# Kernel tuning notes

Hardware: AMD Instinct MI355X
Metric: run time of the kernel (lower is better)

## Reference

```python
import jax, jax.numpy as jnp
import numpy as np

C = 256
NH, NL, NP_ = 8, 3, 4
HD = C // NH
NLAYERS = 6


def sine_pos(H, W, num_feats=128, temperature=10000.0, eps=1e-6):
    # mmdet SinePositionalEncoding with normalize=True and an all-zero padding mask:
    # cumsum of ones -> (i+1), normalized by last element (H or W) * 2*pi.
    scale = 2.0 * np.pi
    y = (jnp.arange(1, H + 1, dtype=jnp.float32) / (H + eps)) * scale
    x = (jnp.arange(1, W + 1, dtype=jnp.float32) / (W + eps)) * scale
    d = jnp.arange(num_feats, dtype=jnp.float32)
    dim_t = temperature ** (2.0 * jnp.floor(d / 2.0) / num_feats)

    def interleave(p):  # p: (n, num_feats) -> sin on even dims, cos on odd dims, interleaved
        return jnp.stack([jnp.sin(p[:, 0::2]), jnp.cos(p[:, 1::2])], axis=-1).reshape(p.shape[0], -1)

    py = interleave(y[:, None] / dim_t)  # (H, num_feats)
    px = interleave(x[:, None] / dim_t)  # (W, num_feats)
    pos = jnp.concatenate([jnp.broadcast_to(py[:, None, :], (H, W, num_feats)),
                           jnp.broadcast_to(px[None, :, :], (H, W, num_feats))], axis=-1)
    return pos.reshape(H * W, 2 * num_feats)


def ref_points(H, W):
    # normalized pixel centers, (x, y) order, shape (H*W, 2)
    ry = (jnp.arange(H, dtype=jnp.float32) + 0.5) / H
    rx = (jnp.arange(W, dtype=jnp.float32) + 0.5) / W
    gy, gx = jnp.meshgrid(ry, rx, indexing='ij')
    return jnp.stack([gx.ravel(), gy.ravel()], axis=-1)


def ln(x, w, b, eps=1e-5):
    m = x.mean(-1, keepdims=True)
    v = x.var(-1, keepdims=True)
    return (x - m) / jnp.sqrt(v + eps) * w + b


def gnorm(x, w, b, groups=32, eps=1e-5):
    B, Ch, H, W = x.shape
    xg = x.reshape(B, groups, Ch // groups, H, W)
    m = xg.mean((2, 3, 4), keepdims=True)
    v = xg.var((2, 3, 4), keepdims=True)
    xg = (xg - m) / jnp.sqrt(v + eps)
    return xg.reshape(B, Ch, H, W) * w[None, :, None, None] + b[None, :, None, None]


def conv3x3(x, w):
    return jax.lax.conv_general_dilated(x, w, (1, 1), 'SAME',
                                        dimension_numbers=('NCHW', 'OIHW', 'NCHW'))


def ms_deform(value, shapes, loc, aw):
    # value (B,S,NH,HD); loc (B,L,NH,NL,NP,2) normalized [0,1]; aw (B,L,NH,NL,NP)
    # Matches F.grid_sample(..., align_corners=False, padding_mode='zeros').
    B, S, nH, hd = value.shape
    Lq, nP = loc.shape[1], loc.shape[4]
    out = jnp.zeros((B, Lq, nH, hd), value.dtype)
    start = 0
    for lvl, (H, W) in enumerate(shapes):
        v = value[:, start:start + H * W].transpose(0, 2, 1, 3)  # (B,nH,HW,hd)
        start += H * W
        l = loc[:, :, :, lvl]                 # (B,Lq,nH,nP,2)
        px = l[..., 0] * W - 0.5
        py = l[..., 1] * H - 0.5
        x0 = jnp.floor(px); y0 = jnp.floor(py)
        lx = px - x0; ly = py - y0
        x0i = x0.astype(jnp.int32); y0i = y0.astype(jnp.int32)

        def tw(w_):  # (B,Lq,nH,nP) -> (B,nH,Lq*nP,1)
            return w_.transpose(0, 2, 1, 3).reshape(B, nH, Lq * nP, 1)

        def gather(xi, yi):
            valid = ((xi >= 0) & (xi < W) & (yi >= 0) & (yi < H)).astype(value.dtype)
            idx = jnp.clip(yi, 0, H - 1) * W + jnp.clip(xi, 0, W - 1)
            idx = idx.transpose(0, 2, 1, 3).reshape(B, nH, Lq * nP)
            g = jnp.take_along_axis(v, idx[..., None], axis=2)  # (B,nH,Lq*nP,hd)
            return g * tw(valid)

        samp = (gather(x0i, y0i) * tw((1 - lx) * (1 - ly))
                + gather(x0i + 1, y0i) * tw(lx * (1 - ly))
                + gather(x0i, y0i + 1) * tw((1 - lx) * ly)
                + gather(x0i + 1, y0i + 1) * tw(lx * ly))
        samp = samp.reshape(B, nH, Lq, nP, hd)
        out = out + jnp.einsum('bqhp,bhqpd->bqhd', aw[:, :, :, lvl], samp)
    return out.reshape(B, Lq, nH * hd)


def _forward(feat0, feat1, feat2, in0_w, in0_b, in1_w, in1_b, in2_w, in2_b,
             off_w, off_b, aw_w, aw_b, vp_w, vp_b, op_w, op_b,
             n1_w, n1_b, ff1_w, ff1_b, ff2_w, ff2_b, n2_w, n2_b,
             fn_w, fn_b, lat_w, lat_b, out_w, gnw, gnb):
    feats = [feat0, feat1, feat2]
    in_ws = [in0_w, in1_w, in2_w]; in_bs = [in0_b, in1_b, in2_b]
    B = feat0.shape[0]
    mlvl = [jnp.einsum('oi,bihw->bohw', w, f) + b[None, :, None, None]
            for f, w, b in zip(feats, in_ws, in_bs)]
    shapes = [(f.shape[2], f.shape[3]) for f in mlvl]
    src = jnp.concatenate([f.reshape(B, C, -1).transpose(0, 2, 1) for f in mlvl], axis=1)  # (B,L,C)
    pos = jnp.concatenate([sine_pos(H, W) for (H, W) in shapes], axis=0)[None]  # (1,L,C)
    ref = jnp.concatenate([ref_points(H, W) for (H, W) in shapes], axis=0)      # (L,2)
    L = ref.shape[0]
    ref = jnp.broadcast_to(ref[None, :, None, :], (B, L, NL, 2))
    norm = jnp.array([[w_, h_] for (h_, w_) in shapes], dtype=src.dtype)  # (NL,2) = (W,H)
    for i in range(NLAYERS):
        q = src + pos
        off = (q @ off_w[i].T + off_b[i]).reshape(B, L, NH, NL, NP_, 2)
        aw = jax.nn.softmax((q @ aw_w[i].T + aw_b[i]).reshape(B, L, NH, NL * NP_), axis=-1)
        aw = aw.reshape(B, L, NH, NL, NP_)
        value = (src @ vp_w[i].T + vp_b[i]).reshape(B, L, NH, HD)
        loc = ref[:, :, None, :, None, :] + off / norm[None, None, None, :, None, :]
        attn = ms_deform(value, shapes, loc, aw) @ op_w[i].T + op_b[i]
        src = ln(src + attn, n1_w[i], n1_b[i])
        ff = jax.nn.relu(src @ ff1_w[i].T + ff1_b[i]) @ ff2_w[i].T + ff2_b[i]
        src = ln(src + ff, n2_w[i], n2_b[i])
    src = ln(src, fn_w, fn_b)
    mems, s = [], 0
    for (H, W) in shapes:
        mems.append(src[:, s:s + H * W].transpose(0, 2, 1).reshape(B, C, H, W))
        s += H * W
    mf = jnp.einsum('oi,bihw->bohw', lat_w, mems[0]) + lat_b[None, :, None, None]
    for i in range(3):
        mf = jax.nn.relu(gnorm(conv3x3(mf, out_w[i]), gnw[i], gnb[i]))
    return (mf, mems[0], mems[1], mems[2])


def setup_inputs():
    ks = iter(jax.random.split(jax.random.key(0), 64))

    def rn(shape, s=0.02):
        return jax.random.normal(next(ks), shape, dtype=jnp.float32) * s

    return dict(
        feat0=rn((1, 256, 64, 64), 1.0),
        feat1=rn((1, 512, 32, 32), 1.0),
        feat2=rn((1, 1024, 16, 16), 1.0),
        in0_w=rn((256, 256)), in0_b=rn((256,)),
        in1_w=rn((256, 512)), in1_b=rn((256,)),
        in2_w=rn((256, 1024)), in2_b=rn((256,)),
        off_w=rn((6, 192, 256), 0.002), off_b=rn((6, 192), 0.5),
        aw_w=rn((6, 96, 256)), aw_b=jnp.zeros((6, 96), jnp.float32),
        vp_w=rn((6, 256, 256)), vp_b=rn((6, 256)),
        op_w=rn((6, 256, 256)), op_b=rn((6, 256)),
        n1_w=jnp.ones((6, 256), jnp.float32), n1_b=jnp.zeros((6, 256), jnp.float32),
        ff1_w=rn((6, 1024, 256)), ff1_b=rn((6, 1024)),
        ff2_w=rn((6, 256, 1024)), ff2_b=rn((6, 256)),
        n2_w=jnp.ones((6, 256), jnp.float32), n2_b=jnp.zeros((6, 256), jnp.float32),
        fn_w=jnp.ones((256,), jnp.float32), fn_b=jnp.zeros((256,), jnp.float32),
        lat_w=rn((256, 256)), lat_b=rn((256,)),
        out_w=rn((3, 256, 256, 3, 3)),
        gnw=jnp.ones((3, 256), jnp.float32), gnb=jnp.zeros((3, 256), jnp.float32),
    )


def reference(feat0, feat1, feat2, in0_w, in0_b, in1_w, in1_b, in2_w, in2_b,
              off_w, off_b, aw_w, aw_b, vp_w, vp_b, op_w, op_b,
              n1_w, n1_b, ff1_w, ff1_b, ff2_w, ff2_b, n2_w, n2_b,
              fn_w, fn_b, lat_w, lat_b, out_w, gnw, gnb):
    return _forward(feat0, feat1, feat2, in0_w, in0_b, in1_w, in1_b, in2_w, in2_b,
                    off_w, off_b, aw_w, aw_b, vp_w, vp_b, op_w, op_b,
                    n1_w, n1_b, ff1_w, ff1_b, ff2_w, ff2_b, n2_w, n2_b,
                    fn_w, fn_b, lat_w, lat_b, out_w, gnw, gnb)
```

## Files before the change

kernel.cpp:

```cpp
#include <hip/hip_runtime.h>
#include <math.h>

#define LTOT 5376

typedef __attribute__((ext_vector_type(8))) __bf16 bf16x8;
typedef __attribute__((ext_vector_type(4))) float f32x4;
typedef __attribute__((ext_vector_type(8))) unsigned short us8;
typedef __attribute__((ext_vector_type(4))) unsigned short us4;

static __device__ __forceinline__ float4 ld4(const float* p) { return *(const float4*)p; }

static __device__ __forceinline__ unsigned short f2bf(float f) {
    unsigned int u = __float_as_uint(f);
    return (unsigned short)((u + 0x7fffu + ((u >> 16) & 1u)) >> 16);
}
static __device__ __forceinline__ float bf2f(unsigned short s) {
    return __uint_as_float(((unsigned int)s) << 16);
}

static __device__ __forceinline__ void gl16(const unsigned short* g, unsigned short* l) {
    __builtin_amdgcn_global_load_lds(
        (const __attribute__((address_space(1))) unsigned int*)g,
        (__attribute__((address_space(3))) unsigned int*)l, 16, 0, 0);
}

__device__ __forceinline__ void gemm_core(
    const unsigned short* __restrict__ A,
    const unsigned short* __restrict__ B,
    const float* __restrict__ bias,
    float* __restrict__ C1, unsigned short* __restrict__ C2,
    const float* __restrict__ posf, unsigned short* __restrict__ qb,
    unsigned short* As, unsigned short* Bs,
    int m0, int mo0, int n0, int N, int K, int omode, int relu)
{
    const int tid  = threadIdx.x;
    const int wave = tid >> 6;
    const int lane = tid & 63;
    const int wm   = (wave >> 1) * 32;
    const int wn   = (wave & 1) * 32;
    const int fr   = lane & 15;
    const int ko   = lane >> 4;

    const int q0 = tid, q1 = tid + 256;
    const int r0 = q0 >> 3, c0v = (q0 & 7) ^ (r0 & 7);
    const int r1 = q1 >> 3, c1v = (q1 & 7) ^ (r1 & 7);
    const unsigned short* a0 = A + (size_t)(m0 + r0) * K + (c0v << 3);
    const unsigned short* a1 = A + (size_t)(m0 + r1) * K + (c1v << 3);
    int bn0 = n0 + r0; if (bn0 > N - 1) bn0 = N - 1;
    int bn1 = n0 + r1; if (bn1 > N - 1) bn1 = N - 1;
    const unsigned short* b0 = B + (size_t)bn0 * K + (c0v << 3);
    const unsigned short* b1 = B + (size_t)bn1 * K + (c1v << 3);
    const int wb = wave << 9;

    f32x4 acc[2][2] = {};
    const int nt = K >> 6;

    auto stage = [&](int buf, int t) {
        const int kof = t << 6;
        gl16(a0 + kof, As + buf * 4096 + wb);
        gl16(a1 + kof, As + buf * 4096 + 2048 + wb);
        gl16(b0 + kof, Bs + buf * 4096 + wb);
        gl16(b1 + kof, Bs + buf * 4096 + 2048 + wb);
    };

    stage(0, 0);
    stage(1, 1);
    asm volatile("s_waitcnt vmcnt(4)" ::: "memory");
    __builtin_amdgcn_s_barrier();
    __builtin_amdgcn_sched_barrier(0);

    for (int t = 0; t < nt; t++) {
        if (t + 2 < nt) stage((t + 2) % 3, t + 2);
        const unsigned short* Ab = As + (t % 3) * 4096;
        const unsigned short* Bb = Bs + (t % 3) * 4096;
        #pragma unroll
        for (int sub = 0; sub < 2; sub++) {
            bf16x8 af[2], bfr[2];
            const int kk = (sub << 2) + ko;
            #pragma unroll
            for (int i = 0; i < 2; i++) {
                int r = wm + i * 16 + fr;
                af[i] = *(const bf16x8*)&Ab[(r << 6) + ((kk ^ (r & 7)) << 3)];
                int c = wn + i * 16 + fr;
                bfr[i] = *(const bf16x8*)&Bb[(c << 6) + ((kk ^ (c & 7)) << 3)];
            }
            #pragma unroll
            for (int i = 0; i < 2; i++)
                #pragma unroll
                for (int j = 0; j < 2; j++)
                    acc[i][j] = __builtin_amdgcn_mfma_f32_16x16x32_bf16(af[i], bfr[j], acc[i][j], 0, 0, 0);
        }
        if (t + 1 < nt) {
            if (t + 2 < nt) asm volatile("s_waitcnt vmcnt(4) lgkmcnt(0)" ::: "memory");
            else            asm volatile("s_waitcnt vmcnt(0) lgkmcnt(0)" ::: "memory");
            __builtin_amdgcn_s_barrier();
            __builtin_amdgcn_sched_barrier(0);
        }
    }

    #pragma unroll
    for (int j = 0; j < 2; j++) {
        int col = n0 + wn + j * 16 + fr;
        if (col >= N) continue;
        float cb = bias[col];
        #pragma unroll
        for (int i = 0; i < 2; i++) {
            #pragma unroll
            for (int r = 0; r < 4; r++) {
                int row = mo0 + wm + i * 16 + ko * 4 + r;
                float v = acc[i][j][r] + cb;
                if (relu) v = fmaxf(v, 0.f);
                size_t off = (size_t)row * N + col;
                if (omode == 0)      C1[off] = v;
                else if (omode == 1) C2[off] = f2bf(v);
                else if (omode == 2) { C1[off] = v; C2[off] = f2bf(v); }
                else { C1[off] = v; C2[off] = f2bf(v); qb[off] = f2bf(v + posf[off]); }
            }
        }
    }
}

__global__ __launch_bounds__(256) void bgemm_k(
    const unsigned short* __restrict__ A, const unsigned short* __restrict__ B,
    const float* __restrict__ bias, float* __restrict__ C1, unsigned short* __restrict__ C2,
    int N, int K, int omode, int relu)
{
    __shared__ unsigned short As[3 * 4096], Bs[3 * 4096];
    int m = blockIdx.y * 64;
    gemm_core(A, B, bias, C1, C2, nullptr, nullptr, As, Bs, m, m, blockIdx.x * 64, N, K, omode, relu);
}

__global__ __launch_bounds__(256) void oavp_k(
    const unsigned short* __restrict__ qbb, const unsigned short* __restrict__ woa,
    const float* __restrict__ boa, float* __restrict__ oab,
    const unsigned short* __restrict__ srcb, const unsigned short* __restrict__ wvp,
    const float* __restrict__ bvp, unsigned short* __restrict__ valb)
{
    __shared__ unsigned short As[3 * 4096], Bs[3 * 4096];
    const int bx = blockIdx.x;
    const int m = blockIdx.y * 64;
    if (bx < 5)
        gemm_core(qbb,  woa, boa, oab, nullptr, nullptr, nullptr, As, Bs, m, m, bx * 64, 288, 256, 0, 0);
    else
        gemm_core(srcb, wvp, bvp, nullptr, valb, nullptr, nullptr, As, Bs, m, m, (bx - 5) * 64, 256, 256, 1, 0);
}

__global__ __launch_bounds__(256) void inproj_k(
    const unsigned short* __restrict__ fT0, const unsigned short* __restrict__ w0, const float* __restrict__ b0,
    const unsigned short* __restrict__ fT1, const unsigned short* __restrict__ w1, const float* __restrict__ b1,
    const unsigned short* __restrict__ fT2, const unsigned short* __restrict__ w2, const float* __restrict__ b2,
    float* __restrict__ src, unsigned short* __restrict__ srcb,
    const float* __restrict__ posf, unsigned short* __restrict__ qbb)
{
    __shared__ unsigned short As[3 * 4096], Bs[3 * 4096];
    const int by = blockIdx.y;
    const int n0 = blockIdx.x * 64;
    if (by < 64)
        gemm_core(fT0, w0, b0, src, srcb, posf, qbb, As, Bs, by * 64, by * 64, n0, 256, 256, 3, 0);
    else if (by < 80)
        gemm_core(fT1, w1, b1, src, srcb, posf, qbb, As, Bs, (by - 64) * 64, 4096 + (by - 64) * 64, n0, 256, 512, 3, 0);
    else
        gemm_core(fT2, w2, b2, src, srcb, posf, qbb, As, Bs, (by - 80) * 64, 5120 + (by - 80) * 64, n0, 256, 1024, 3, 0);
}

__global__ __launch_bounds__(256) void setup_k(
    const float* __restrict__ off_w, const float* __restrict__ off_b,
    const float* __restrict__ aw_w,  const float* __restrict__ aw_b,
    unsigned short* __restrict__ w_oa, float* __restrict__ b_oa,
    const float* __restrict__ out_w, unsigned short* __restrict__ wcb,
    const float* __restrict__ s0, const float* __restrict__ s1,
    const float* __restrict__ s2, const float* __restrict__ s3,
    const float* __restrict__ s4, const float* __restrict__ s5,
    const float* __restrict__ s6, const float* __restrict__ s7,
    unsigned short* __restrict__ dcvt,
    float* __restrict__ pos)
{
    const int bid = blockIdx.x;
    const int tid = threadIdx.x;
    if (bid < 1728) {
        int idx = bid * 256 + tid;
        int i = idx / 73728;
        int r = idx - i * 73728;
        int n = r >> 8;
        int k = r & 255;
        float v = (n < 192) ? off_w[((size_t)i * 192 + n) * 256 + k]
                            : aw_w[((size_t)i * 96 + (n - 192)) * 256 + k];
        w_oa[idx] = f2bf(v);
        if (k == 0)
            b_oa[i * 288 + n] = (n < 192) ? off_b[i * 192 + n] : aw_b[i * 96 + (n - 192)];
    } else if (bid < 8640) {
        int idx = (bid - 1728) * 256 + tid;
        int c   = idx / 589824;
        int r   = idx - c * 589824;
        int icc = r / 73728;
        int r2  = r - icc * 73728;
        int oc  = r2 / 288;
        int r3  = r2 - oc * 288;
        int tap = r3 >> 5;
        int sl  = r3 & 31;
        int ic  = icc * 32 + (((sl >> 3) ^ ((oc >> 1) & 3)) << 3) + (sl & 7);
        wcb[idx] = f2bf(out_w[(((size_t)(c * 256 + oc)) * 256 + ic) * 9 + tap]);
    } else if (bid < 12992) {
        int i = (bid - 8640) * 256 + tid;
        const float* s; int off;
        if      (i <   98304) { s = s0; off = 0; }
        else if (i <  196608) { s = s1; off = 98304; }
        else if (i <  589824) { s = s2; off = 196608; }
        else if (i <  983040) { s = s3; off = 589824; }
        else if (i <  999424) { s = s4; off = 983040; }
        else if (i < 1032192) { s = s5; off = 999424; }
        else if (i < 1097728) { s = s6; off = 1032192; }
        else                  { s = s7; off = 1097728; }
        float4 v = ld4(&s[(size_t)(i - off) << 2]);
        us4 r = { f2bf(v.x), f2bf(v.y), f2bf(v.z), f2bf(v.w) };
        *(us4*)&dcvt[(size_t)i << 2] = r;
    } else {
        int idx = (bid - 12992) * 256 + tid;
        int l = idx >> 7;
        int pr = idx & 127;
        int half = pr >> 6;
        int j = pr & 63;
        int HW, sh, p;
        if (l < 4096)      { HW = 64; sh = 6; p = l; }
        else if (l < 5120) { HW = 32; sh = 5; p = l - 4096; }
        else               { HW = 16; sh = 4; p = l - 5120; }
        int y = p >> sh;
        int x = p & (HW - 1);
        float invT = exp2f((float)j * (-13.287712379549449f / 64.f));
        float coord = (half == 0) ? (float)(y + 1) : (float)(x + 1);
        float v = coord / ((float)HW + 1e-6f) * 6.283185307179586f;
        float arg = v * invT;
        size_t base = (size_t)l * 256 + half * 128 + (j << 1);
        pos[base]     = sinf(arg);
        pos[base + 1] = cosf(arg);
    }
}

__global__ void cvtT3_k(const float* __restrict__ f0, const float* __restrict__ f1,
                        const float* __restrict__ f2,
                        unsigned short* __restrict__ d0, unsigned short* __restrict__ d1,
                        unsigned short* __restrict__ d2)
{
    __shared__ float t[32][33];
    const int bid = blockIdx.x;
    const float* src; unsigned short* dst; int Ci, P, bx, by;
    if (bid < 1024)      { src = f0; dst = d0; Ci = 256;  P = 4096; bx = bid & 127;        by = bid >> 7; }
    else if (bid < 1536) { src = f1; dst = d1; Ci = 512;  P = 1024; bx = (bid - 1024) & 31; by = (bid - 1024) >> 5; }
    else                 { src = f2; dst = d2; Ci = 1024; P = 256;  bx = (bid - 1536) & 7;  by = (bid - 1536) >> 3; }
    int c0 = by * 32, p0 = bx * 32;
    int x = threadIdx.x, y = threadIdx.y;
    for (int i = y; i < 32; i += 8)
        t[i][x] = src[(size_t)(c0 + i) * P + p0 + x];
    __syncthreads();
    for (int i = y; i < 32; i += 8)
        dst[(size_t)(p0 + i) * Ci + c0 + x] = f2bf(t[x][i]);
}

__global__ __launch_bounds__(256) void msdef_k(
    const unsigned short* __restrict__ valb, const float* __restrict__ oab,
    unsigned short* __restrict__ out)
{
    __shared__ float sw[8 * 288];
    const int tid = threadIdx.x;
    const int bl = blockIdx.x;
    #pragma unroll
    for (int id = tid; id < 576; id += 256)
        ((float4*)sw)[id] = ((const float4*)(oab + (size_t)bl * 2304))[id];
    __syncthreads();

    const int p = tid >> 5;
    const int t = tid & 31;
    const int l = bl * 8 + p;
    const int h = t >> 2;
    const int co = (t & 3) << 3;
    const float* mo = sw + p * 288;

    float aw_r[12];
    {
        const float* sc = mo + 192 + h * 12;
        float mx = -1e30f;
        #pragma unroll
        for (int j = 0; j < 12; j++) { aw_r[j] = sc[j]; mx = fmaxf(mx, aw_r[j]); }
        float su = 0.f;
        #pragma unroll
        for (int j = 0; j < 12; j++) { aw_r[j] = expf(aw_r[j] - mx); su += aw_r[j]; }
        float inv = 1.f / su;
        #pragma unroll
        for (int j = 0; j < 12; j++) aw_r[j] *= inv;
    }

    float rx, ry;
    {
        int HW, sh, q;
        if (l < 4096)      { HW = 64; sh = 6; q = l; }
        else if (l < 5120) { HW = 32; sh = 5; q = l - 4096; }
        else               { HW = 16; sh = 4; q = l - 5120; }
        int y = q >> sh;
        int x = q & (HW - 1);
        rx = (x + 0.5f) / (float)HW;
        ry = (y + 0.5f) / (float)HW;
    }

    const int starts[3] = {0, 4096, 5120};
    const int dims[3]   = {64, 32, 16};
    float acc[8] = {};
    #pragma unroll
    for (int s = 0; s < 3; s++) {
        const int D = dims[s];
        const int st = starts[s];
        #pragma unroll
        for (int pt = 0; pt < 4; pt++) {
            float a  = aw_r[(s << 2) + pt];
            float px = rx * D + mo[h * 24 + (s << 3) + (pt << 1)]     - 0.5f;
            float py = ry * D + mo[h * 24 + (s << 3) + (pt << 1) + 1] - 0.5f;
            float x0f = floorf(px), y0f = floorf(py);
            float lx = px - x0f, ly = py - y0f;
            int x0 = (int)x0f, y0 = (int)y0f;
            float w00 = a * (1.f - lx) * (1.f - ly);
            float w10 = a * lx * (1.f - ly);
            float w01 = a * (1.f - lx) * ly;
            float w11 = a * lx * ly;
            #pragma unroll
            for (int cy = 0; cy < 2; cy++) {
                int yi = y0 + cy;
                if (yi < 0 || yi >= D) continue;
                #pragma unroll
                for (int cx = 0; cx < 2; cx++) {
                    int xi = x0 + cx;
                    if (xi < 0 || xi >= D) continue;
                    float w = cy ? (cx ? w11 : w01) : (cx ? w10 : w00);
                    us8 v = *(const us8*)&valb[((size_t)(st + yi * D + xi) << 8) + (h << 5) + co];
                    #pragma unroll
                    for (int e = 0; e < 8; e++)
                        acc[e] = fmaf(w, bf2f(v[e]), acc[e]);
                }
            }
        }
    }
    us8 r;
    #pragma unroll
    for (int e = 0; e < 8; e++) r[e] = f2bf(acc[e]);
    *(us8*)&out[((size_t)l << 8) + (h << 5) + co] = r;
}

template<bool HAS_ADD, bool HAS_POS>
__global__ __launch_bounds__(256) void ln_k(float* __restrict__ src, const float* __restrict__ add,
                                            const float* __restrict__ w, const float* __restrict__ b,
                                            unsigned short* __restrict__ outb,
                                            const float* __restrict__ posf,
                                            unsigned short* __restrict__ qbout)
{
    int row = blockIdx.x * 4 + (threadIdx.x >> 6);
    int lane = threadIdx.x & 63;
    size_t base = (size_t)row * 256 + (lane << 2);
    float4 x = ld4(&src[base]);
    if (HAS_ADD) {
        float4 a = ld4(&add[base]);
        x.x += a.x; x.y += a.y; x.z += a.z; x.w += a.w;
    }
    float s = x.x + x.y + x.z + x.w;
    #pragma unroll
    for (int o = 32; o > 0; o >>= 1) s += __shfl_xor(s, o, 64);
    float m = s * (1.f / 256.f);
    float d0 = x.x - m, d1 = x.y - m, d2 = x.z - m, d3 = x.w - m;
    float v = d0 * d0 + d1 * d1 + d2 * d2 + d3 * d3;
    #pragma unroll
    for (int o = 32; o > 0; o >>= 1) v += __shfl_xor(v, o, 64);
    float rs = rsqrtf(v * (1.f / 256.f) + 1e-5f);
    float4 wv = ld4(&w[lane << 2]);
    float4 bv = ld4(&b[lane << 2]);
    float4 o4;
    o4.x = d0 * rs * wv.x + bv.x;
    o4.y = d1 * rs * wv.y + bv.y;
    o4.z = d2 * rs * wv.z + bv.z;
    o4.w = d3 * rs * wv.w + bv.w;
    *(float4*)&src[base] = o4;
    us4 r = { f2bf(o4.x), f2bf(o4.y), f2bf(o4.z), f2bf(o4.w) };
    *(us4*)&outb[base] = r;
    if (HAS_POS) {
        float4 p4 = ld4(&posf[base]);
        us4 q = { f2bf(o4.x + p4.x), f2bf(o4.y + p4.y), f2bf(o4.z + p4.z), f2bf(o4.w + p4.w) };
        *(us4*)&qbout[base] = q;
    }
}

__global__ void tr3_k(const float* __restrict__ src, float* __restrict__ out)
{
    __shared__ float t[32][33];
    const int bx = blockIdx.x;
    const float* s; float* d; int HW, p0;
    if (bx < 128)      { s = src;           d = out;            HW = 4096; p0 = bx * 32; }
    else if (bx < 160) { s = src + 1048576; d = out + 1048576;  HW = 1024; p0 = (bx - 128) * 32; }
    else               { s = src + 1310720; d = out + 1310720;  HW = 256;  p0 = (bx - 160) * 32; }
    int c0 = blockIdx.y * 32;
    int x = threadIdx.x, y = threadIdx.y;
    for (int i = y; i < 32; i += 8)
        t[i][x] = s[(size_t)(p0 + i) * 256 + c0 + x];
    __syncthreads();
    for (int i = y; i < 32; i += 8)
        d[(size_t)(c0 + i) * HW + p0 + x] = t[x][i];
}

__global__ __launch_bounds__(256) void conv3b_k(const unsigned short* __restrict__ inb,
                                                const unsigned short* __restrict__ wcb,
                                                float* __restrict__ out)
{
    __shared__ __align__(16) unsigned char smem[43776];
    unsigned short* sIn = (unsigned short*)smem;
    unsigned short* sW  = (unsigned short*)(smem + 6912);
    float* sO = (float*)smem;

    const int tid = threadIdx.x;
    const int mb = blockIdx.x;
    const int y0 = (mb >> 2) << 2;
    const int x0 = (mb & 3) << 4;
    const int oc0 = blockIdx.y << 6;
    const int wave = tid >> 6, lane = tid & 63;
    const int wm = (wave >> 1) * 32, wn = (wave & 1) * 32;
    const int fr = lane & 15, ko = lane >> 4;

    f32x4 acc[2][2] = {};

    for (int icc = 0; icc < 8; icc++) {
        __syncthreads();
        #pragma unroll
        for (int id = tid; id < 432; id += 256) {
            int pxi = id >> 2, ch = id & 3;
            int r = pxi / 18, s = pxi - r * 18;
            int gy = y0 - 1 + r, gx = x0 - 1 + s;
            us8 v = {};
            if (gy >= 0 && gy < 64 && gx >= 0 && gx < 64)
                v = *(const us8*)&inb[((size_t)(gy * 64 + gx) << 8) + (icc << 5) + (ch << 3)];
            *(us8*)&sIn[(pxi << 5) + ((ch ^ ((s >> 1) & 3)) << 3)] = v;
        }
        const unsigned short* wsrc = wcb + (((size_t)icc * 256 + oc0) * 9 << 5);
        #pragma unroll
        for (int id = tid; id < 2304; id += 256)
            *(us8*)&sW[id << 3] = *(const us8*)&wsrc[id << 3];
        __syncthreads();

        #pragma unroll
        for (int tap = 0; tap < 9; tap++) {
            const int ky = tap / 3, kx = tap - ky * 3;
            bf16x8 a[2], b[2];
            #pragma unroll
            for (int i = 0; i < 2; i++) {
                int px = wm + i * 16 + fr;
                int r = (px >> 4) + ky;
                int s = (px & 15) + kx;
                a[i] = *(const bf16x8*)&sIn[(((r * 18 + s)) << 5) + ((ko ^ ((s >> 1) & 3)) << 3)];
            }
            #pragma unroll
            for (int j = 0; j < 2; j++) {
                int oc = wn + j * 16 + fr;
                b[j] = *(const bf16x8*)&sW[(((oc * 9) + tap) << 5) + ((ko ^ ((oc >> 1) & 3)) << 3)];
            }
            #pragma unroll
            for (int i = 0; i < 2; i++)
                #pragma unroll
                for (int j = 0; j < 2; j++)
                    acc[i][j] = __builtin_amdgcn_mfma_f32_16x16x32_bf16(a[i], b[j], acc[i][j], 0, 0, 0);
        }
    }

    __syncthreads();
    #pragma unroll
    for (int i = 0; i < 2; i++)
        #pragma unroll
        for (int j = 0; j < 2; j++) {
            int oc = wn + j * 16 + fr;
            int pxb = wm + i * 16 + ko * 4;
            *(f32x4*)&sO[oc * 68 + pxb] = acc[i][j];
        }
    __syncthreads();
    {
        int oc_r = tid >> 2, yy = tid & 3;
        float* dst = &out[(size_t)(oc0 + oc_r) * 4096 + (y0 + yy) * 64 + x0];
        const float* srcl = &sO[oc_r * 68 + yy * 16];
        #pragma unroll
        for (int q = 0; q < 4; q++)
            *(float4*)&dst[q * 4] = *(const float4*)&srcl[q * 4];
    }
}

__global__ __launch_bounds__(256) void gnstats_k(const float* __restrict__ x, float* __restrict__ st)
{
    int g = blockIdx.x;
    const float* p = x + (size_t)g * 8 * 4096;
    float s = 0.f, ss = 0.f;
    for (int i = threadIdx.x * 4; i < 32768; i += 1024) {
        float4 v = ld4(&p[i]);
        s  += v.x + v.y + v.z + v.w;
        ss += v.x * v.x + v.y * v.y + v.z * v.z + v.w * v.w;
    }
    #pragma unroll
    for (int o = 32; o > 0; o >>= 1) {
        s  += __shfl_xor(s, o, 64);
        ss += __shfl_xor(ss, o, 64);
    }
    __shared__ float rs[4], rss[4];
    int wid = threadIdx.x >> 6;
    if ((threadIdx.x & 63) == 0) { rs[wid] = s; rss[wid] = ss; }
    __syncthreads();
    if (threadIdx.x == 0) {
        float S = rs[0] + rs[1] + rs[2] + rs[3];
        float SS = rss[0] + rss[1] + rss[2] + rss[3];
        float m = S * (1.f / 32768.f);
        float var = SS * (1.f / 32768.f) - m * m;
        st[g * 2] = m;
        st[g * 2 + 1] = rsqrtf(var + 1e-5f);
    }
}

__global__ void gnapply_b_k(const float* __restrict__ x, const float* __restrict__ st,
                            const float* __restrict__ w, const float* __restrict__ b,
                            unsigned short* __restrict__ o)
{
    int i = blockIdx.x * blockDim.x + threadIdx.x;
    if (i >= 262144) return;
    int c = i >> 10;
    int g = c >> 3;
    int px0 = (i & 1023) << 2;
    float m = st[g * 2], rs = st[g * 2 + 1];
    float sw = w[c], sb = b[c];
    float4 v = ld4(&x[(size_t)i << 2]);
    float r0 = fmaxf((v.x - m) * rs * sw + sb, 0.f);
    float r1 = fmaxf((v.y - m) * rs * sw + sb, 0.f);
    float r2 = fmaxf((v.z - m) * rs * sw + sb, 0.f);
    float r3 = fmaxf((v.w - m) * rs * sw + sb, 0.f);
    o[(size_t)(px0 + 0) * 256 + c] = f2bf(r0);
    o[(size_t)(px0 + 1) * 256 + c] = f2bf(r1);
    o[(size_t)(px0 + 2) * 256 + c] = f2bf(r2);
    o[(size_t)(px0 + 3) * 256 + c] = f2bf(r3);
}

__global__ void gnapply_f_k(const float* __restrict__ x, const float* __restrict__ st,
                            const float* __restrict__ w, const float* __restrict__ b,
                            float* __restrict__ o)
{
    int i = blockIdx.x * blockDim.x + threadIdx.x;
    if (i >= 262144) return;
    int c = i >> 10;
    int g = c >> 3;
    float m = st[g * 2], rs = st[g * 2 + 1];
    float sw = w[c], sb = b[c];
    float4 v = ld4(&x[(size_t)i << 2]);
    float4 r;
    r.x = fmaxf((v.x - m) * rs * sw + sb, 0.f);
    r.y = fmaxf((v.y - m) * rs * sw + sb, 0.f);
    r.z = fmaxf((v.z - m) * rs * sw + sb, 0.f);
    r.w = fmaxf((v.w - m) * rs * sw + sb, 0.f);
    *(float4*)&o[(size_t)i << 2] = r;
}

extern "C" void kernel_launch(void* const* d_in, const int* in_sizes, int n_in,
                              void* d_out, int out_size, void* d_ws, size_t ws_size,
                              hipStream_t stream)
{
    (void)in_sizes; (void)n_in; (void)out_size; (void)ws_size;
    const float* feat0 = (const float*)d_in[0];
    const float* feat1 = (const float*)d_in[1];
    const float* feat2 = (const float*)d_in[2];
    const float* in0_w = (const float*)d_in[3];
    const float* in0_b = (const float*)d_in[4];
    const float* in1_w = (const float*)d_in[5];
    const float* in1_b = (const float*)d_in[6];
    const float* in2_w = (const float*)d_in[7];
    const float* in2_b = (const float*)d_in[8];
    const float* off_w = (const float*)d_in[9];
    const float* off_b = (const float*)d_in[10];
    const float* aw_w  = (const float*)d_in[11];
    const float* aw_b  = (const float*)d_in[12];
    const float* vp_w  = (const float*)d_in[13];
    const float* vp_b  = (const float*)d_in[14];
    const float* op_w  = (const float*)d_in[15];
    const float* op_b  = (const float*)d_in[16];
    const float* n1_w  = (const float*)d_in[17];
    const float* n1_b  = (const float*)d_in[18];
    const float* ff1_w = (const float*)d_in[19];
    const float* ff1_b = (const float*)d_in[20];
    const float* ff2_w = (const float*)d_in[21];
    const float* ff2_b = (const float*)d_in[22];
    const float* n2_w  = (const float*)d_in[23];
    const float* n2_b  = (const float*)d_in[24];
    const float* fn_w  = (const float*)d_in[25];
    const float* fn_b  = (const float*)d_in[26];
    const float* lat_w = (const float*)d_in[27];
    const float* lat_b = (const float*)d_in[28];
    const float* out_w = (const float*)d_in[29];
    const float* gnw   = (const float*)d_in[30];
    const float* gnb   = (const float*)d_in[31];
    float* out = (float*)d_out;

    float* ws     = (float*)d_ws;
    float* src    = ws;
    float* pos    = src  + 1376256;
    float* tmp    = pos  + 1376256;
    float* valbuf = tmp  + 1376256;
    float* oab    = valbuf + 1376256;
    float* stats  = oab  + 1548288;
    float* boa    = stats + 64;
    float* pong   = pos;

    unsigned short* valb = (unsigned short*)valbuf;
    unsigned short* latb = (unsigned short*)(valbuf + 688128);

    unsigned short* ub = (unsigned short*)(boa + 1728);
    unsigned short* srcb  = ub; ub += 1376256;
    unsigned short* qbb   = ub; ub += 1376256;
    unsigned short* msdb  = ub; ub += 1376256;
    unsigned short* ffhb  = ub; ub += 5505024;
    unsigned short* w_oa  = ub; ub += 442368;
    unsigned short* w_vp  = ub; ub += 393216;
    unsigned short* w_op  = ub; ub += 393216;
    unsigned short* w_ff1 = ub; ub += 1572864;
    unsigned short* w_ff2 = ub; ub += 1572864;
    unsigned short* w_in0 = ub; ub += 65536;
    unsigned short* w_in1 = ub; ub += 131072;
    unsigned short* w_in2 = ub; ub += 262144;
    unsigned short* w_lat = ub; ub += 65536;
    unsigned short* wcb   = ub; ub += 1769472;

    unsigned short* fT0 = ffhb;
    unsigned short* fT1 = ffhb + 1048576;
    unsigned short* fT2 = ffhb + 1572864;
    unsigned short* pingb = qbb;

    setup_k<<<15680, 256, 0, stream>>>(off_w, off_b, aw_w, aw_b, w_oa, boa,
                                       out_w, wcb,
                                       vp_w, op_w, ff1_w, ff2_w, in0_w, in1_w, in2_w, lat_w, w_vp,
                                       pos);
    cvtT3_k<<<1792, dim3(32, 8), 0, stream>>>(feat0, feat1, feat2, fT0, fT1, fT2);

    inproj_k<<<dim3(4, 84), 256, 0, stream>>>(fT0, w_in0, in0_b, fT1, w_in1, in1_b,
                                              fT2, w_in2, in2_b, src, srcb, pos, qbb);

    for (int i = 0; i < 6; i++) {
        oavp_k<<<dim3(9, 84), 256, 0, stream>>>(qbb, w_oa + i*73728, boa + i*288, oab,
                                                srcb, w_vp + i*65536, vp_b + i*256, valb);
        msdef_k<<<672, 256, 0, stream>>>(valb, oab, msdb);
        bgemm_k<<<dim3(4, 84), 256, 0, stream>>>(msdb, w_op + i*65536, op_b + i*256, tmp, nullptr, 256, 256, 0, 0);
        ln_k<true,false><<<1344, 256, 0, stream>>>(src, tmp, n1_w + i*256, n1_b + i*256, srcb, nullptr, nullptr);
        bgemm_k<<<dim3(16, 84), 256, 0, stream>>>(srcb, w_ff1 + i*262144, ff1_b + i*1024, nullptr, ffhb, 1024, 256, 1, 1);
        bgemm_k<<<dim3(4, 84), 256, 0, stream>>>(ffhb, w_ff2 + i*262144, ff2_b + i*256, tmp, nullptr, 256, 1024, 0, 0);
        if (i < 5)
            ln_k<true,true><<<1344, 256, 0, stream>>>(src, tmp, n2_w + i*256, n2_b + i*256, srcb, pos, qbb);
        else
            ln_k<true,false><<<1344, 256, 0, stream>>>(src, tmp, n2_w + i*256, n2_b + i*256, srcb, nullptr, nullptr);
    }
    ln_k<false,false><<<1344, 256, 0, stream>>>(src, nullptr, fn_w, fn_b, srcb, nullptr, nullptr);

    tr3_k<<<dim3(168, 8), dim3(32, 8), 0, stream>>>(src, out + 1048576);

    bgemm_k<<<dim3(4, 64), 256, 0, stream>>>(srcb, w_lat, lat_b, nullptr, latb, 256, 256, 1, 0);

    conv3b_k<<<dim3(64,4), 256, 0, stream>>>(latb, wcb, pong);
    gnstats_k<<<32, 256, 0, stream>>>(pong, stats);
    gnapply_b_k<<<1024, 256, 0, stream>>>(pong, stats, gnw, gnb, pingb);

    conv3b_k<<<dim3(64,4), 256, 0, stream>>>(pingb, wcb + 589824, pong);
    gnstats_k<<<32, 256, 0, stream>>>(pong, stats);
    gnapply_b_k<<<1024, 256, 0, stream>>>(pong, stats, gnw + 256, gnb + 256, pingb);

    conv3b_k<<<dim3(64,4), 256, 0, stream>>>(pingb, wcb + 1179648, pong);
    gnstats_k<<<32, 256, 0, stream>>>(pong, stats);
    gnapply_f_k<<<1024, 256, 0, stream>>>(pong, stats, gnw + 512, gnb + 512, out);
}
```

Before: 617.8 us.

## Fuse setup/transpose, final layernorms, tail transpose+lateral GEMM, and groupnorm stats/apply

Folds the feature transpose into the setup kernel and fuses the last layer's norm2 with the final norm. It also merges the output transpose and lateral GEMM into one launch and combines group-norm stats and apply into a single 1024-thread kernel per group. The 3x3 conv is retiled to 32 output channels per block, doubling the grid and shrinking shared memory. The aim is fewer kernel launches and more parallelism in the conv tail. The cost is a group-norm pass that runs only 32 blocks and smaller MFMA tiles per wave.

```diff
diff --git a/kernel.cpp b/kernel.cpp
--- a/kernel.cpp
+++ b/kernel.cpp
@@ -173,7 +173,9 @@
     const float* __restrict__ s4, const float* __restrict__ s5,
     const float* __restrict__ s6, const float* __restrict__ s7,
     unsigned short* __restrict__ dcvt,
-    float* __restrict__ pos)
+    float* __restrict__ pos,
+    const float* __restrict__ f0, const float* __restrict__ f1, const float* __restrict__ f2,
+    unsigned short* __restrict__ d0, unsigned short* __restrict__ d1, unsigned short* __restrict__ d2)
 {
     const int bid = blockIdx.x;
     const int tid = threadIdx.x;
@@ -214,7 +216,7 @@
         float4 v = ld4(&s[(size_t)(i - off) << 2]);
         us4 r = { f2bf(v.x), f2bf(v.y), f2bf(v.z), f2bf(v.w) };
         *(us4*)&dcvt[(size_t)i << 2] = r;
-    } else {
+    } else if (bid < 15680) {
         int idx = (bid - 12992) * 256 + tid;
         int l = idx >> 7;
         int pr = idx & 127;
@@ -233,27 +235,21 @@
         size_t base = (size_t)l * 256 + half * 128 + (j << 1);
         pos[base]     = sinf(arg);
         pos[base + 1] = cosf(arg);
-    }
-}
-
-__global__ void cvtT3_k(const float* __restrict__ f0, const float* __restrict__ f1,
-                        const float* __restrict__ f2,
-                        unsigned short* __restrict__ d0, unsigned short* __restrict__ d1,
-                        unsigned short* __restrict__ d2)
-{
-    __shared__ float t[32][33];
-    const int bid = blockIdx.x;
-    const float* src; unsigned short* dst; int Ci, P, bx, by;
-    if (bid < 1024)      { src = f0; dst = d0; Ci = 256;  P = 4096; bx = bid & 127;        by = bid >> 7; }
-    else if (bid < 1536) { src = f1; dst = d1; Ci = 512;  P = 1024; bx = (bid - 1024) & 31; by = (bid - 1024) >> 5; }
-    else                 { src = f2; dst = d2; Ci = 1024; P = 256;  bx = (bid - 1536) & 7;  by = (bid - 1536) >> 3; }
-    int c0 = by * 32, p0 = bx * 32;
-    int x = threadIdx.x, y = threadIdx.y;
-    for (int i = y; i < 32; i += 8)
-        t[i][x] = src[(size_t)(c0 + i) * P + p0 + x];
-    __syncthreads();
-    for (int i = y; i < 32; i += 8)
-        dst[(size_t)(p0 + i) * Ci + c0 + x] = f2bf(t[x][i]);
+    } else {
+        __shared__ float t[32][33];
+        int b = bid - 15680;
+        const float* src; unsigned short* dst; int Ci, P, bx, by;
+        if (b < 1024)      { src = f0; dst = d0; Ci = 256;  P = 4096; bx = b & 127;        by = b >> 7; }
+        else if (b < 1536) { src = f1; dst = d1; Ci = 512;  P = 1024; bx = (b - 1024) & 31; by = (b - 1024) >> 5; }
+        else               { src = f2; dst = d2; Ci = 1024; P = 256;  bx = (b - 1536) & 7;  by = (b - 1536) >> 3; }
+        int c0 = by * 32, p0 = bx * 32;
+        int x = tid & 31, y = tid >> 5;
+        for (int i = y; i < 32; i += 8)
+            t[i][x] = src[(size_t)(c0 + i) * P + p0 + x];
+        __syncthreads();
+        for (int i = y; i < 32; i += 8)
+            dst[(size_t)(p0 + i) * Ci + c0 + x] = f2bf(t[x][i]);
+    }
 }
 
 __global__ __launch_bounds__(256) void msdef_k(
@@ -343,7 +339,7 @@
     *(us8*)&out[((size_t)l << 8) + (h << 5) + co] = r;
 }
 
-template<bool HAS_ADD, bool HAS_POS>
+template<bool HAS_POS>
 __global__ __launch_bounds__(256) void ln_k(float* __restrict__ src, const float* __restrict__ add,
                                             const float* __restrict__ w, const float* __restrict__ b,
                                             unsigned short* __restrict__ outb,
@@ -354,10 +350,8 @@
     int lane = threadIdx.x & 63;
     size_t base = (size_t)row * 256 + (lane << 2);
     float4 x = ld4(&src[base]);
-    if (HAS_ADD) {
-        float4 a = ld4(&add[base]);
-        x.x += a.x; x.y += a.y; x.z += a.z; x.w += a.w;
-    }
+    float4 a = ld4(&add[base]);
+    x.x += a.x; x.y += a.y; x.z += a.z; x.w += a.w;
     float s = x.x + x.y + x.z + x.w;
     #pragma unroll
     for (int o = 32; o > 0; o >>= 1) s += __shfl_xor(s, o, 64);
@@ -384,28 +378,88 @@
     }
 }
 
-__global__ void tr3_k(const float* __restrict__ src, float* __restrict__ out)
-{
-    __shared__ float t[32][33];
-    const int bx = blockIdx.x;
-    const float* s; float* d; int HW, p0;
-    if (bx < 128)      { s = src;           d = out;            HW = 4096; p0 = bx * 32; }
-    else if (bx < 160) { s = src + 1048576; d = out + 1048576;  HW = 1024; p0 = (bx - 128) * 32; }
-    else               { s = src + 1310720; d = out + 1310720;  HW = 256;  p0 = (bx - 160) * 32; }
-    int c0 = blockIdx.y * 32;
-    int x = threadIdx.x, y = threadIdx.y;
-    for (int i = y; i < 32; i += 8)
-        t[i][x] = s[(size_t)(p0 + i) * 256 + c0 + x];
-    __syncthreads();
-    for (int i = y; i < 32; i += 8)
-        d[(size_t)(c0 + i) * HW + p0 + x] = t[x][i];
+__global__ __launch_bounds__(256) void ln2fn_k(float* __restrict__ src, const float* __restrict__ add,
+                                               const float* __restrict__ w2, const float* __restrict__ b2,
+                                               const float* __restrict__ wf, const float* __restrict__ bf,
+                                               unsigned short* __restrict__ outb)
+{
+    int row = blockIdx.x * 4 + (threadIdx.x >> 6);
+    int lane = threadIdx.x & 63;
+    size_t base = (size_t)row * 256 + (lane << 2);
+    float4 x = ld4(&src[base]);
+    float4 a = ld4(&add[base]);
+    x.x += a.x; x.y += a.y; x.z += a.z; x.w += a.w;
+    float s = x.x + x.y + x.z + x.w;
+    #pragma unroll
+    for (int o = 32; o > 0; o >>= 1) s += __shfl_xor(s, o, 64);
+    float m = s * (1.f / 256.f);
+    float d0 = x.x - m, d1 = x.y - m, d2 = x.z - m, d3 = x.w - m;
+    float v = d0 * d0 + d1 * d1 + d2 * d2 + d3 * d3;
+    #pragma unroll
+    for (int o = 32; o > 0; o >>= 1) v += __shfl_xor(v, o, 64);
+    float rs = rsqrtf(v * (1.f / 256.f) + 1e-5f);
+    float4 wv = ld4(&w2[lane << 2]);
+    float4 bv = ld4(&b2[lane << 2]);
+    float4 o4;
+    o4.x = d0 * rs * wv.x + bv.x;
+    o4.y = d1 * rs * wv.y + bv.y;
+    o4.z = d2 * rs * wv.z + bv.z;
+    o4.w = d3 * rs * wv.w + bv.w;
+    float s2 = o4.x + o4.y + o4.z + o4.w;
+    #pragma unroll
+    for (int o = 32; o > 0; o >>= 1) s2 += __shfl_xor(s2, o, 64);
+    float m2 = s2 * (1.f / 256.f);
+    float e0 = o4.x - m2, e1 = o4.y - m2, e2 = o4.z - m2, e3 = o4.w - m2;
+    float v2 = e0 * e0 + e1 * e1 + e2 * e2 + e3 * e3;
+    #pragma unroll
+    for (int o = 32; o > 0; o >>= 1) v2 += __shfl_xor(v2, o, 64);
+    float rs2 = rsqrtf(v2 * (1.f / 256.f) + 1e-5f);
+    float4 wf4 = ld4(&wf[lane << 2]);
+    float4 bf4 = ld4(&bf[lane << 2]);
+    float4 o5;
+    o5.x = e0 * rs2 * wf4.x + bf4.x;
+    o5.y = e1 * rs2 * wf4.y + bf4.y;
+    o5.z = e2 * rs2 * wf4.z + bf4.z;
+    o5.w = e3 * rs2 * wf4.w + bf4.w;
+    *(float4*)&src[base] = o5;
+    us4 r = { f2bf(o5.x), f2bf(o5.y), f2bf(o5.z), f2bf(o5.w) };
+    *(us4*)&outb[base] = r;
+}
+
+__global__ __launch_bounds__(256) void tail_k(
+    const float* __restrict__ src, float* __restrict__ outb_,
+    const unsigned short* __restrict__ srcb, const unsigned short* __restrict__ w_lat,
+    const float* __restrict__ lat_b, unsigned short* __restrict__ latb)
+{
+    if (blockIdx.x < 1344) {
+        __shared__ float t[32][33];
+        int b = blockIdx.x;
+        int bx = b % 168, cy = b / 168;
+        const float* s; float* d; int HW, p0;
+        if (bx < 128)      { s = src;           d = outb_;           HW = 4096; p0 = bx * 32; }
+        else if (bx < 160) { s = src + 1048576; d = outb_ + 1048576; HW = 1024; p0 = (bx - 128) * 32; }
+        else               { s = src + 1310720; d = outb_ + 1310720; HW = 256;  p0 = (bx - 160) * 32; }
+        int c0 = cy * 32;
+        int x = threadIdx.x & 31, y = threadIdx.x >> 5;
+        for (int i = y; i < 32; i += 8)
+            t[i][x] = s[(size_t)(p0 + i) * 256 + c0 + x];
+        __syncthreads();
+        for (int i = y; i < 32; i += 8)
+            d[(size_t)(c0 + i) * HW + p0 + x] = t[x][i];
+    } else {
+        __shared__ unsigned short As[3 * 4096], Bs[3 * 4096];
+        int b = blockIdx.x - 1344;
+        int m = (b >> 2) * 64;
+        gemm_core(srcb, w_lat, lat_b, nullptr, latb, nullptr, nullptr, As, Bs,
+                  m, m, (b & 3) * 64, 256, 256, 1, 0);
+    }
 }
 
 __global__ __launch_bounds__(256) void conv3b_k(const unsigned short* __restrict__ inb,
                                                 const unsigned short* __restrict__ wcb,
                                                 float* __restrict__ out)
 {
-    __shared__ __align__(16) unsigned char smem[43776];
+    __shared__ __align__(16) unsigned char smem[25344];
     unsigned short* sIn = (unsigned short*)smem;
     unsigned short* sW  = (unsigned short*)(smem + 6912);
     float* sO = (float*)smem;
@@ -414,12 +468,13 @@
     const int mb = blockIdx.x;
     const int y0 = (mb >> 2) << 2;
     const int x0 = (mb & 3) << 4;
-    const int oc0 = blockIdx.y << 6;
+    const int oc0 = blockIdx.y << 5;
     const int wave = tid >> 6, lane = tid & 63;
-    const int wm = (wave >> 1) * 32, wn = (wave & 1) * 32;
+    const int wm = (wave >> 1) * 32;
+    const int wn = (wave & 1) * 16;
     const int fr = lane & 15, ko = lane >> 4;
 
-    f32x4 acc[2][2] = {};
+    f32x4 acc[2] = {};
 
     for (int icc = 0; icc < 8; icc++) {
         __syncthreads();
@@ -435,14 +490,14 @@
         }
         const unsigned short* wsrc = wcb + (((size_t)icc * 256 + oc0) * 9 << 5);
         #pragma unroll
-        for (int id = tid; id < 2304; id += 256)
+        for (int id = tid; id < 1152; id += 256)
             *(us8*)&sW[id << 3] = *(const us8*)&wsrc[id << 3];
         __syncthreads();
 
         #pragma unroll
         for (int tap = 0; tap < 9; tap++) {
             const int ky = tap / 3, kx = tap - ky * 3;
-            bf16x8 a[2], b[2];
+            bf16x8 a[2], b;
             #pragma unroll
             for (int i = 0; i < 2; i++) {
                 int px = wm + i * 16 + fr;
@@ -450,45 +505,44 @@
                 int s = (px & 15) + kx;
                 a[i] = *(const bf16x8*)&sIn[(((r * 18 + s)) << 5) + ((ko ^ ((s >> 1) & 3)) << 3)];
             }
-            #pragma unroll
-            for (int j = 0; j < 2; j++) {
-                int oc = wn + j * 16 + fr;
-                b[j] = *(const bf16x8*)&sW[(((oc * 9) + tap) << 5) + ((ko ^ ((oc >> 1) & 3)) << 3)];
+            {
+                int oc = wn + fr;
+                b = *(const bf16x8*)&sW[(((oc * 9) + tap) << 5) + ((ko ^ ((oc >> 1) & 3)) << 3)];
             }
             #pragma unroll
             for (int i = 0; i < 2; i++)
-                #pragma unroll
-                for (int j = 0; j < 2; j++)
-                    acc[i][j] = __builtin_amdgcn_mfma_f32_16x16x32_bf16(a[i], b[j], acc[i][j], 0, 0, 0);
+                acc[i] = __builtin_amdgcn_mfma_f32_16x16x32_bf16(a[i], b, acc[i], 0, 0, 0);
         }
     }
 
     __syncthreads();
     #pragma unroll
-    for (int i = 0; i < 2; i++)
-        #pragma unroll
-        for (int j = 0; j < 2; j++) {
-            int oc = wn + j * 16 + fr;
-            int pxb = wm + i * 16 + ko * 4;
-            *(f32x4*)&sO[oc * 68 + pxb] = acc[i][j];
-        }
+    for (int i = 0; i < 2; i++) {
+        int oc = wn + fr;
+        int pxb = wm + i * 16 + ko * 4;
+        *(f32x4*)&sO[oc * 68 + pxb] = acc[i];
+    }
     __syncthreads();
     {
-        int oc_r = tid >> 2, yy = tid & 3;
-        float* dst = &out[(size_t)(oc0 + oc_r) * 4096 + (y0 + yy) * 64 + x0];
-        const float* srcl = &sO[oc_r * 68 + yy * 16];
-        #pragma unroll
-        for (int q = 0; q < 4; q++)
-            *(float4*)&dst[q * 4] = *(const float4*)&srcl[q * 4];
-    }
-}
-
-__global__ __launch_bounds__(256) void gnstats_k(const float* __restrict__ x, float* __restrict__ st)
-{
-    int g = blockIdx.x;
-    const float* p = x + (size_t)g * 8 * 4096;
+        int oc_r = tid >> 3;
+        int yy   = (tid >> 1) & 3;
+        int xh   = (tid & 1) << 3;
+        float* dst = &out[(size_t)(oc0 + oc_r) * 4096 + (y0 + yy) * 64 + x0 + xh];
+        const float* srcl = &sO[oc_r * 68 + yy * 16 + xh];
+        *(float4*)&dst[0] = *(const float4*)&srcl[0];
+        *(float4*)&dst[4] = *(const float4*)&srcl[4];
+    }
+}
+
+template<int OUT>
+__global__ __launch_bounds__(1024) void gn_k(const float* __restrict__ x,
+                                             const float* __restrict__ w, const float* __restrict__ b,
+                                             unsigned short* __restrict__ ob, float* __restrict__ of)
+{
+    const int g = blockIdx.x;
+    const float* p = x + (size_t)g * 32768;
     float s = 0.f, ss = 0.f;
-    for (int i = threadIdx.x * 4; i < 32768; i += 1024) {
+    for (int i = threadIdx.x * 4; i < 32768; i += 4096) {
         float4 v = ld4(&p[i]);
         s  += v.x + v.y + v.z + v.w;
         ss += v.x * v.x + v.y * v.y + v.z * v.z + v.w * v.w;
@@ -498,59 +552,36 @@
         s  += __shfl_xor(s, o, 64);
         ss += __shfl_xor(ss, o, 64);
     }
-    __shared__ float rs[4], rss[4];
+    __shared__ float rs[16], rss[16];
     int wid = threadIdx.x >> 6;
     if ((threadIdx.x & 63) == 0) { rs[wid] = s; rss[wid] = ss; }
     __syncthreads();
-    if (threadIdx.x == 0) {
-        float S = rs[0] + rs[1] + rs[2] + rs[3];
-        float SS = rss[0] + rss[1] + rss[2] + rss[3];
-        float m = S * (1.f / 32768.f);
-        float var = SS * (1.f / 32768.f) - m * m;
-        st[g * 2] = m;
-        st[g * 2 + 1] = rsqrtf(var + 1e-5f);
-    }
-}
-
-__global__ void gnapply_b_k(const float* __restrict__ x, const float* __restrict__ st,
-                            const float* __restrict__ w, const float* __restrict__ b,
-                            unsigned short* __restrict__ o)
-{
-    int i = blockIdx.x * blockDim.x + threadIdx.x;
-    if (i >= 262144) return;
-    int c = i >> 10;
-    int g = c >> 3;
-    int px0 = (i & 1023) << 2;
-    float m = st[g * 2], rs = st[g * 2 + 1];
-    float sw = w[c], sb = b[c];
-    float4 v = ld4(&x[(size_t)i << 2]);
-    float r0 = fmaxf((v.x - m) * rs * sw + sb, 0.f);
-    float r1 = fmaxf((v.y - m) * rs * sw + sb, 0.f);
-    float r2 = fmaxf((v.z - m) * rs * sw + sb, 0.f);
-    float r3 = fmaxf((v.w - m) * rs * sw + sb, 0.f);
-    o[(size_t)(px0 + 0) * 256 + c] = f2bf(r0);
-    o[(size_t)(px0 + 1) * 256 + c] = f2bf(r1);
-    o[(size_t)(px0 + 2) * 256 + c] = f2bf(r2);
-    o[(size_t)(px0 + 3) * 256 + c] = f2bf(r3);
-}
-
-__global__ void gnapply_f_k(const float* __restrict__ x, const float* __restrict__ st,
-                            const float* __restrict__ w, const float* __restrict__ b,
-                            float* __restrict__ o)
-{
-    int i = blockIdx.x * blockDim.x + threadIdx.x;
-    if (i >= 262144) return;
-    int c = i >> 10;
-    int g = c >> 3;
-    float m = st[g * 2], rs = st[g * 2 + 1];
-    float sw = w[c], sb = b[c];
-    float4 v = ld4(&x[(size_t)i << 2]);
-    float4 r;
-    r.x = fmaxf((v.x - m) * rs * sw + sb, 0.f);
-    r.y = fmaxf((v.y - m) * rs * sw + sb, 0.f);
-    r.z = fmaxf((v.z - m) * rs * sw + sb, 0.f);
-    r.w = fmaxf((v.w - m) * rs * sw + sb, 0.f);
-    *(float4*)&o[(size_t)i << 2] = r;
+    float S = 0.f, SS = 0.f;
+    #pragma unroll
+    for (int k = 0; k < 16; k++) { S += rs[k]; SS += rss[k]; }
+    float m = S * (1.f / 32768.f);
+    float rstd = rsqrtf(SS * (1.f / 32768.f) - m * m + 1e-5f);
+
+    for (int i = threadIdx.x; i < 8192; i += 1024) {
+        int cl = i >> 10;
+        int c = (g << 3) + cl;
+        float sw = w[c], sb = b[c];
+        float4 v = ld4(&p[(size_t)i << 2]);
+        float r0 = fmaxf((v.x - m) * rstd * sw + sb, 0.f);
+        float r1 = fmaxf((v.y - m) * rstd * sw + sb, 0.f);
+        float r2 = fmaxf((v.z - m) * rstd * sw + sb, 0.f);
+        float r3 = fmaxf((v.w - m) * rstd * sw + sb, 0.f);
+        if (OUT == 0) {
+            int px0 = (i & 1023) << 2;
+            ob[(size_t)(px0 + 0) * 256 + c] = f2bf(r0);
+            ob[(size_t)(px0 + 1) * 256 + c] = f2bf(r1);
+            ob[(size_t)(px0 + 2) * 256 + c] = f2bf(r2);
+            ob[(size_t)(px0 + 3) * 256 + c] = f2bf(r3);
+        } else {
+            float4 r = make_float4(r0, r1, r2, r3);
+            *(float4*)&of[(size_t)g * 32768 + ((size_t)i << 2)] = r;
+        }
+    }
 }
 
 extern "C" void kernel_launch(void* const* d_in, const int* in_sizes, int n_in,
@@ -626,11 +657,11 @@
     unsigned short* fT2 = ffhb + 1572864;
     unsigned short* pingb = qbb;
 
-    setup_k<<<15680, 256, 0, stream>>>(off_w, off_b, aw_w, aw_b, w_oa, boa,
+    setup_k<<<17472, 256, 0, stream>>>(off_w, off_b, aw_w, aw_b, w_oa, boa,
                                        out_w, wcb,
                                        vp_w, op_w, ff1_w, ff2_w, in0_w, in1_w, in2_w, lat_w, w_vp,
-                                       pos);
-    cvtT3_k<<<1792, dim3(32, 8), 0, stream>>>(feat0, feat1, feat2, fT0, fT1, fT2);
+                                       pos,
+                                       feat0, feat1, feat2, fT0, fT1, fT2);
 
     inproj_k<<<dim3(4, 84), 256, 0, stream>>>(fT0, w_in0, in0_b, fT1, w_in1, in1_b,
                                               fT2, w_in2, in2_b, src, srcb, pos, qbb);
@@ -640,29 +671,23 @@
                                                 srcb, w_vp + i*65536, vp_b + i*256, valb);
         msdef_k<<<672, 256, 0, stream>>>(valb, oab, msdb);
         bgemm_k<<<dim3(4, 84), 256, 0, stream>>>(msdb, w_op + i*65536, op_b + i*256, tmp, nullptr, 256, 256, 0, 0);
-        ln_k<true,false><<<1344, 256, 0, stream>>>(src, tmp, n1_w + i*256, n1_b + i*256, srcb, nullptr, nullptr);
+        ln_k<false><<<1344, 256, 0, stream>>>(src, tmp, n1_w + i*256, n1_b + i*256, srcb, nullptr, nullptr);
         bgemm_k<<<dim3(16, 84), 256, 0, stream>>>(srcb, w_ff1 + i*262144, ff1_b + i*1024, nullptr, ffhb, 1024, 256, 1, 1);
         bgemm_k<<<dim3(4, 84), 256, 0, stream>>>(ffhb, w_ff2 + i*262144, ff2_b + i*256, tmp, nullptr, 256, 1024, 0, 0);
         if (i < 5)
-            ln_k<true,true><<<1344, 256, 0, stream>>>(src, tmp, n2_w + i*256, n2_b + i*256, srcb, pos, qbb);
+            ln_k<true><<<1344, 256, 0, stream>>>(src, tmp, n2_w + i*256, n2_b + i*256, srcb, pos, qbb);
         else
-            ln_k<true,false><<<1344, 256, 0, stream>>>(src, tmp, n2_w + i*256, n2_b + i*256, srcb, nullptr, nullptr);
-    }
-    ln_k<false,false><<<1344, 256, 0, stream>>>(src, nullptr, fn_w, fn_b, srcb, nullptr, nullptr);
-
-    tr3_k<<<dim3(168, 8), dim3(32, 8), 0, stream>>>(src, out + 1048576);
-
-    bgemm_k<<<dim3(4, 64), 256, 0, stream>>>(srcb, w_lat, lat_b, nullptr, latb, 256, 256, 1, 0);
-
-    conv3b_k<<<dim3(64,4), 256, 0, stream>>>(latb, wcb, pong);
-    gnstats_k<<<32, 256, 0, stream>>>(pong, stats);
-    gnapply_b_k<<<1024, 256, 0, stream>>>(pong, stats, gnw, gnb, pingb);
-
-    conv3b_k<<<dim3(64,4), 256, 0, stream>>>(pingb, wcb + 589824, pong);
-    gnstats_k<<<32, 256, 0, stream>>>(pong, stats);
-    gnapply_b_k<<<1024, 256, 0, stream>>>(pong, stats, gnw + 256, gnb + 256, pingb);
-
-    conv3b_k<<<dim3(64,4), 256, 0, stream>>>(pingb, wcb + 1179648, pong);
-    gnstats_k<<<32, 256, 0, stream>>>(pong, stats);
-    gnapply_f_k<<<1024, 256, 0, stream>>>(pong, stats, gnw + 512, gnb + 512, out);
-}
+            ln2fn_k<<<1344, 256, 0, stream>>>(src, tmp, n2_w + i*256, n2_b + i*256, fn_w, fn_b, srcb);
+    }
+
+    tail_k<<<1600, 256, 0, stream>>>(src, out + 1048576, srcb, w_lat, lat_b, latb);
+
+    conv3b_k<<<dim3(64, 8), 256, 0, stream>>>(latb, wcb, pong);
+    gn_k<0><<<32, 1024, 0, stream>>>(pong, gnw, gnb, pingb, nullptr);
+
+    conv3b_k<<<dim3(64, 8), 256, 0, stream>>>(pingb, wcb + 589824, pong);
+    gn_k<0><<<32, 1024, 0, stream>>>(pong, gnw + 256, gnb + 256, pingb, nullptr);
+
+    conv3b_k<<<dim3(64, 8), 256, 0, stream>>>(pingb, wcb + 1179648, pong);
+    gn_k<1><<<32, 1024, 0, stream>>>(pong, gnw + 512, gnb + 512, nullptr, out);
+}
```

After: 606.0 us (median of 2 runs). About the same (-1.9%).
